# Kernel optimization log

Measured on AMD Instinct MI355X. Metric: run time of the kernel, lower is better.

## Reference

```python
import jax, jax.numpy as jnp
import numpy as np

B, T, DIN, D = 8, 2048, 1024, 1024
EPS = 1e-6


def setup_inputs() -> dict:
    key = jax.random.key(0)
    k0, k1, k2, k3 = jax.random.split(key, 4)
    x = jax.random.normal(k0, (B, T, DIN), dtype=jnp.float32)
    h0 = jax.random.normal(k1, (B, D), dtype=jnp.float32)
    s0 = jax.random.normal(k2, (B, D), dtype=jnp.float32)
    # xavier_uniform for weight [7D, DIN]
    bound = float(np.sqrt(6.0 / (DIN + 7 * D)))
    W = jax.random.uniform(k3, (7 * D, DIN), dtype=jnp.float32, minval=-bound, maxval=bound)
    # structured bias init from _init_weights: [0, 1, 0, 0, 0, 2, 0.5] per block
    b = jnp.concatenate([
        jnp.zeros(D), jnp.ones(D), jnp.zeros(D), jnp.zeros(D),
        jnp.zeros(D), jnp.full((D,), 2.0), jnp.full((D,), 0.5)
    ]).astype(jnp.float32)
    return {"x": x, "h0": h0, "s0": s0, "W": W, "b": b}


def _forward(x, h0, s0, W, b):
    Bv, Tv, _ = x.shape
    Dv = W.shape[0] // 7
    gates = (jnp.einsum('bti,oi->bto', x, W) + b).reshape(Bv, Tv, 7, Dv)
    r, z, k, v, h_pre, decay, alpha = (gates[:, :, i] for i in range(7))
    # per-element pairwise RMS norms, exactly as in the Triton kernel
    rms_control = jnp.sqrt((r * r + z * z) / 2 + EPS)
    rms_kv = jnp.sqrt((k * k + v * v) / 2 + EPS)
    # r is normalized+sigmoided in the kernel but never used -> no effect on output
    z = jax.nn.sigmoid(z / rms_control)
    decay = jax.nn.sigmoid(decay / jnp.sqrt(decay * decay + EPS))
    alpha = jax.nn.sigmoid(alpha / jnp.sqrt(alpha * alpha + EPS))
    h_pre = h_pre / jnp.sqrt(h_pre * h_pre + EPS)
    kv = (k / rms_kv) * (v / rms_kv) / (rms_kv * rms_kv + EPS)
    # time-major [T,B,D] for the scan
    seq = tuple(jnp.swapaxes(a, 0, 1) for a in (z, kv, h_pre, decay, alpha))

    def step(carry, ins):
        h, s = carry
        z_t, kv_t, hp_t, d_t, a_t = ins
        s = d_t * s + a_t * kv_t
        c = jax.nn.sigmoid(2.0 * (hp_t + s)) * 2.0 - 1.0
        h = (1.0 - z_t) * c + z_t * h
        return (h, s), h

    (_, sT), out = jax.lax.scan(step, (h0, s0), seq)
    return jnp.swapaxes(out, 0, 1), sT  # ([B,T,D], [B,D])


def reference(x, h0, s0, W, b):
    return _forward(x, h0, s0, W, b)
```

## Files before the change

kernel.cpp:

```cpp
#include <hip/hip_runtime.h>
#include <hip/hip_bf16.h>

typedef _Float16 f16x8 __attribute__((ext_vector_type(8)));
typedef float f32x4 __attribute__((ext_vector_type(4)));

static constexpr int BB = 8;
static constexpr int TT = 2048;
static constexpr int DD = 1024;
static constexpr int MM = BB * TT;
static constexpr int NN = 7 * DD;
static constexpr int APS = 2048;
static constexpr int NCSUB = 32;
static constexpr int LC = TT / NCSUB;
static constexpr int BD = BB * DD;
#define EPS_ 1e-6f

static constexpr size_t SZ_CMP = (size_t)MM * DD * 8;
static constexpr size_t SZ_BP  = (size_t)NN * 3072 * 2;
static constexpr size_t SZ_SM  = (size_t)NCSUB * BD * 4;
static constexpr size_t OFF_BP  = SZ_CMP;
static constexpr size_t OFF_SM  = OFF_BP + SZ_BP;
static constexpr size_t OFF_AP  = OFF_SM + 6 * SZ_SM;
static constexpr size_t CHUNK_BYTES = (size_t)MM * 18432;

__device__ __forceinline__ unsigned short bf_rne(float f) {
    unsigned u = __builtin_bit_cast(unsigned, f);
    unsigned r = (u + 0x7fffu + ((u >> 16) & 1u)) >> 16;
    return (unsigned short)r;
}
__device__ __forceinline__ float bf2f(unsigned short u) {
    return __builtin_bit_cast(float, ((unsigned)u) << 16);
}
__device__ __forceinline__ float f16f(unsigned short u) {
    return (float)__builtin_bit_cast(_Float16, u);
}
__device__ __forceinline__ unsigned short f16b(float f) {
    return __builtin_bit_cast(unsigned short, (_Float16)f);
}
__device__ __forceinline__ float sigm(float x) { return 1.0f / (1.0f + __expf(-x)); }

typedef __attribute__((address_space(3))) void lds_void;
typedef const __attribute__((address_space(1))) void gbl_void;
__device__ __forceinline__ void gload16(const void* g, void* l) {
    __builtin_amdgcn_global_load_lds((gbl_void*)g, (lds_void*)l, 16, 0, 0);
}

__global__ __launch_bounds__(256) void prep_w(const float* __restrict__ W,
                                              _Float16* __restrict__ Bp1,
                                              _Float16* __restrict__ Bp2) {
    int i = blockIdx.x * 256 + threadIdx.x;
    int o = i >> 10, k = i & 1023;
    int g = o >> 10, d = o & 1023;
    float wv = W[i] * 512.0f;
    _Float16 w1 = (_Float16)wv;
    _Float16 w2 = (_Float16)(wv - (float)w1);
    if (g == 0 || g == 1 || g == 4) {
        int r1 = (g == 4 ? 2 : g) * 1024 + d;
        Bp1[(size_t)r1 * 1024 + k] = w1;
    } else {
        int r2 = (g < 4 ? g - 2 : g - 3) * 1024 + d;
        size_t base = (size_t)r2 * 3072 + k;
        Bp2[base] = w1; Bp2[base + 1024] = w1; Bp2[base + 2048] = w2;
    }
}

__global__ __launch_bounds__(256) void prep_x(const float* __restrict__ x,
                                              _Float16* __restrict__ Ap,
                                              int tc, int Tc, int tcShift) {
    int i = blockIdx.x * 256 + threadIdx.x;
    int rho = i >> 10, k = i & 1023;
    int b = rho >> tcShift, tau = rho & (Tc - 1);
    size_t m = (size_t)b * TT + (size_t)tc * Tc + tau;
    float xv = x[m * DD + k] * 16.0f;
    _Float16 x1 = (_Float16)xv;
    _Float16 x2 = (_Float16)(xv - (float)x1);
    size_t base = (size_t)rho * APS + k;
    Ap[base] = x1; Ap[base + 1024] = x2;
}

template<int KT, int NTILES, int NCOLS, int KIND>
__global__ __launch_bounds__(512) void gemm_k(const _Float16* __restrict__ Ap,
                                              const _Float16* __restrict__ Bp,
                                              const float* __restrict__ bias,
                                              _Float16* __restrict__ Gc, int Mt) {
    constexpr int KSTR = KT * 64;
    __shared__ __align__(16) _Float16 As[256 * 64];
    __shared__ __align__(16) _Float16 Bs[128 * 64];
    int nwg = Mt * NTILES;
    int bid = blockIdx.x;
    int cpx = nwg >> 3;
    int swz = (bid & 7) * cpx + (bid >> 3);
    int bm = swz / NTILES, bn = swz % NTILES;
    int m0 = bm * 256, n0 = bn * 128;
    int tid = threadIdx.x;
    int w = tid >> 6, l = tid & 63;
    int wm = w >> 1, wn = w & 1;
    int lrow = l & 15, kg = l >> 4;
    f32x4 acc[4][4] = {};
    const char* Ab = (const char*)Ap;
    const char* Bb = (const char*)Bp;
    for (int k0 = 0; k0 < KT * 64; k0 += 64) {
        int ak0 = k0 & 2047;
#pragma unroll
        for (int q = 0; q < 4; ++q) {
            int c = q * 512 + tid;
            int row = c >> 3, sgg = (c & 7) ^ (row & 7);
            gload16(Ab + ((size_t)(m0 + row) * APS + ak0 + sgg * 8) * 2, (char*)As + c * 16);
        }
#pragma unroll
        for (int q = 0; q < 2; ++q) {
            int c = q * 512 + tid;
            int row = c >> 3, sgg = (c & 7) ^ (row & 7);
            gload16(Bb + ((size_t)(n0 + row) * KSTR + k0 + sgg * 8) * 2, (char*)Bs + c * 16);
        }
        __syncthreads();
#pragma unroll
        for (int kk = 0; kk < 64; kk += 32) {
            f16x8 af[4], bfr[4];
            int sgb = kg + (kk >> 3);
#pragma unroll
            for (int i = 0; i < 4; ++i) {
                int r = wm * 64 + i * 16 + lrow;
                af[i] = *(const f16x8*)(As + r * 64 + (size_t)((sgb ^ (r & 7)) * 8));
            }
#pragma unroll
            for (int j = 0; j < 4; ++j) {
                int r = wn * 64 + j * 16 + lrow;
                bfr[j] = *(const f16x8*)(Bs + r * 64 + (size_t)((sgb ^ (r & 7)) * 8));
            }
#pragma unroll
            for (int i = 0; i < 4; ++i)
#pragma unroll
                for (int j = 0; j < 4; ++j)
                    acc[i][j] = __builtin_amdgcn_mfma_f32_16x16x32_f16(af[i], bfr[j], acc[i][j], 0, 0, 0);
        }
        __syncthreads();
    }
    const float inv = 1.0f / 8192.0f;
#pragma unroll
    for (int j = 0; j < 4; ++j) {
        int o = n0 + wn * 64 + j * 16 + lrow;
        int g = o >> 10, d = o & 1023;
        float bv;
        if (KIND == 1) bv = bias[(g == 2 ? 4 : g) * 1024 + d];
        else           bv = bias[(g < 2 ? g + 2 : g + 3) * 1024 + d];
#pragma unroll
        for (int i = 0; i < 4; ++i) {
            int rb = m0 + wm * 64 + i * 16 + kg * 4;
#pragma unroll
            for (int r = 0; r < 4; ++r) {
                float val = acc[i][j][r] * inv + bv;
                if (KIND == 1) {
                    if (g == 2) val = val * rsqrtf(val * val + EPS_);
                } else {
                    if (g >= 2) val = sigm(val * rsqrtf(val * val + EPS_));
                }
                Gc[(size_t)(rb + r) * NCOLS + o] = (_Float16)val;
            }
        }
    }
}

__global__ __launch_bounds__(256) void compact_k(const _Float16* __restrict__ Gc1,
                                                 const _Float16* __restrict__ Gc2,
                                                 ushort2* __restrict__ cmpA,
                                                 ushort2* __restrict__ cmpB,
                                                 int tc, int Tc, int tcShift) {
    int idx = blockIdx.x * 256 + threadIdx.x;
    int rho = idx >> 10, d = idx & 1023;
    const _Float16* row1 = Gc1 + (size_t)rho * 3072;
    const _Float16* row2 = Gc2 + (size_t)rho * 4096;
    float r   = row1[d], z  = row1[1024 + d], hpn = row1[2048 + d];
    float k   = row2[d], v  = row2[1024 + d];
    float ds  = row2[2048 + d], as = row2[3072 + d];
    float rc2 = (r * r + z * z) * 0.5f + EPS_;
    float zs = sigm(z * rsqrtf(rc2));
    float rk2 = (k * k + v * v) * 0.5f + EPS_;
    float kv = (k * v) / (rk2 * (rk2 + EPS_));
    float akv = as * kv;
    int b = rho >> tcShift, tau = rho & (Tc - 1);
    size_t m = (size_t)b * TT + (size_t)tc * Tc + tau;
    ushort2 ua; ua.x = bf_rne(akv); ua.y = f16b(ds);
    ushort2 ub; ub.x = f16b(zs);    ub.y = f16b(hpn);
    cmpA[m * DD + d] = ua;
    cmpB[m * DD + d] = ub;
}

__global__ __launch_bounds__(256) void passA(const ushort2* __restrict__ cmpA,
                                             float* __restrict__ SP, float* __restrict__ SQ) {
    int bid = blockIdx.x;
    int b = bid >> 7, rem = bid & 127;
    int ch = rem >> 2, d = (rem & 3) * 256 + threadIdx.x;
    const ushort2* p = cmpA + ((size_t)(b * TT + ch * LC)) * DD + d;
    float P = 1.0f, Q = 0.0f;
#pragma unroll 4
    for (int i = 0; i < LC; ++i) {
        ushort2 u = p[(size_t)i * DD];
        float akv = bf2f(u.x), ds = f16f(u.y);
        P *= ds; Q = ds * Q + akv;
    }
    int bd = b * DD + d;
    SP[ch * BD + bd] = P; SQ[ch * BD + bd] = Q;
}

__global__ __launch_bounds__(256) void passB(const float* __restrict__ s0,
                                             const float* __restrict__ SP, const float* __restrict__ SQ,
                                             float* __restrict__ Sst, float* __restrict__ sT) {
    int bd = blockIdx.x * 256 + threadIdx.x;
    float s = s0[bd];
    for (int ch = 0; ch < NCSUB; ++ch) {
        Sst[ch * BD + bd] = s;
        s = SP[ch * BD + bd] * s + SQ[ch * BD + bd];
    }
    sT[bd] = s;
}

__global__ __launch_bounds__(256) void passC(const ushort2* __restrict__ cmpA,
                                             const ushort2* __restrict__ cmpB,
                                             const float* __restrict__ Sst,
                                             float* __restrict__ HZ, float* __restrict__ HR) {
    int bid = blockIdx.x;
    int b = bid >> 7, rem = bid & 127;
    int ch = rem >> 2, d = (rem & 3) * 256 + threadIdx.x;
    int bd = b * DD + d;
    float s = Sst[ch * BD + bd];
    float Z = 1.0f, R = 0.0f;
    size_t base = ((size_t)(b * TT + ch * LC)) * DD + d;
#pragma unroll 4
    for (int i = 0; i < LC; ++i) {
        ushort2 ua = cmpA[base + (size_t)i * DD];
        ushort2 ub = cmpB[base + (size_t)i * DD];
        float akv = bf2f(ua.x), ds = f16f(ua.y), zs = f16f(ub.x), hpn = f16f(ub.y);
        s = ds * s + akv;
        float c = 2.0f * sigm(2.0f * (hpn + s)) - 1.0f;
        Z *= zs; R = zs * R + (1.0f - zs) * c;
    }
    HZ[ch * BD + bd] = Z; HR[ch * BD + bd] = R;
}

__global__ __launch_bounds__(256) void passD(const float* __restrict__ h0,
                                             const float* __restrict__ HZ, const float* __restrict__ HR,
                                             float* __restrict__ Hst) {
    int bd = blockIdx.x * 256 + threadIdx.x;
    float h = h0[bd];
    for (int ch = 0; ch < NCSUB; ++ch) {
        Hst[ch * BD + bd] = h;
        h = HZ[ch * BD + bd] * h + HR[ch * BD + bd];
    }
}

__global__ __launch_bounds__(256) void passE(const ushort2* __restrict__ cmpA,
                                             const ushort2* __restrict__ cmpB,
                                             const float* __restrict__ Sst,
                                             const float* __restrict__ Hst,
                                             float* __restrict__ out) {
    int bid = blockIdx.x;
    int b = bid >> 7, rem = bid & 127;
    int ch = rem >> 2, d = (rem & 3) * 256 + threadIdx.x;
    int bd = b * DD + d;
    float s = Sst[ch * BD + bd];
    float h = Hst[ch * BD + bd];
    size_t base = ((size_t)(b * TT + ch * LC)) * DD + d;
    float* op = out + base;
#pragma unroll 4
    for (int i = 0; i < LC; ++i) {
        ushort2 ua = cmpA[base + (size_t)i * DD];
        ushort2 ub = cmpB[base + (size_t)i * DD];
        float akv = bf2f(ua.x), ds = f16f(ua.y), zs = f16f(ub.x), hpn = f16f(ub.y);
        s = ds * s + akv;
        float c = 2.0f * sigm(2.0f * (hpn + s)) - 1.0f;
        h = (1.0f - zs) * c + zs * h;
        op[(size_t)i * DD] = h;
    }
}

__global__ __launch_bounds__(256) void sentinel_k(float* __restrict__ sT) {
    int i = blockIdx.x * 256 + threadIdx.x;
    if (i < BD) sT[i] = 1e9f;
}

extern "C" void kernel_launch(void* const* d_in, const int* in_sizes, int n_in,
                              void* d_out, int out_size, void* d_ws, size_t ws_size,
                              hipStream_t stream) {
    const float* x    = (const float*)d_in[0];
    const float* h0   = (const float*)d_in[1];
    const float* s0   = (const float*)d_in[2];
    const float* W    = (const float*)d_in[3];
    const float* bias = (const float*)d_in[4];
    float* out = (float*)d_out;
    float* sT  = out + (size_t)MM * DD;
    char* ws = (char*)d_ws;

    int NCH = 0;
    for (int c : {2, 4, 8, 16, 32}) {
        if (OFF_AP + CHUNK_BYTES / c <= ws_size) { NCH = c; break; }
    }
    if (!NCH) {
        sentinel_k<<<BD / 256, 256, 0, stream>>>(sT);
        return;
    }
    int Mc = MM / NCH;
    int Tc = TT / NCH;
    int tcShift = 31 - __builtin_clz(Tc);
    int Mt = Mc / 256;

    ushort2* cmpA = (ushort2*)ws;
    ushort2* cmpB = (ushort2*)(ws + (size_t)MM * DD * 4);
    _Float16* Bp1 = (_Float16*)(ws + OFF_BP);
    _Float16* Bp2 = (_Float16*)(ws + OFF_BP + (size_t)3072 * 1024 * 2);
    float* SP  = (float*)(ws + OFF_SM);
    float* SQ  = (float*)(ws + OFF_SM + 1 * SZ_SM);
    float* Sst = (float*)(ws + OFF_SM + 2 * SZ_SM);
    float* HZ  = (float*)(ws + OFF_SM + 3 * SZ_SM);
    float* HR  = (float*)(ws + OFF_SM + 4 * SZ_SM);
    float* Hst = (float*)(ws + OFF_SM + 5 * SZ_SM);
    _Float16* Ap  = (_Float16*)(ws + OFF_AP);
    _Float16* Gc1 = (_Float16*)(ws + OFF_AP + (size_t)Mc * APS * 2);
    _Float16* Gc2 = Gc1 + (size_t)Mc * 3072;

    prep_w<<<(NN * DD) / 256, 256, 0, stream>>>(W, Bp1, Bp2);
    for (int tc = 0; tc < NCH; ++tc) {
        prep_x<<<Mc * 4, 256, 0, stream>>>(x, Ap, tc, Tc, tcShift);
        gemm_k<16, 24, 3072, 1><<<Mt * 24, 512, 0, stream>>>(Ap, Bp1, bias, Gc1, Mt);
        gemm_k<48, 32, 4096, 2><<<Mt * 32, 512, 0, stream>>>(Ap, Bp2, bias, Gc2, Mt);
        compact_k<<<Mc * 4, 256, 0, stream>>>(Gc1, Gc2, cmpA, cmpB, tc, Tc, tcShift);
    }
    passA<<<BB * NCSUB * 4, 256, 0, stream>>>(cmpA, SP, SQ);
    passB<<<BD / 256, 256, 0, stream>>>(s0, SP, SQ, Sst, sT);
    passC<<<BB * NCSUB * 4, 256, 0, stream>>>(cmpA, cmpB, Sst, HZ, HR);
    passD<<<BD / 256, 256, 0, stream>>>(h0, HZ, HR, Hst);
    passE<<<BB * NCSUB * 4, 256, 0, stream>>>(cmpA, cmpB, Sst, Hst, out);
}
```

Measured before the change: 754.7 us.

## Replace second gate GEMM with 256x256-tile, 8-wave pipelined MFMA kernel

Adds a new gemm8 kernel for the second (k, v, decay, alpha) GEMM. It uses 256x256 output tiles, 8 waves each computing 128x64, a double-buffered 128KB LDS pipeline with direct global-to-LDS loads, XOR-swizzled LDS addressing, s_setprio around MFMA bursts, and an XCD-aware block swizzle. The larger tile raises data reuse per loaded byte and aims to overlap loads with MFMA work. The cost is one workgroup per CU, high register pressure and fewer workgroups to fill the device.

```diff
diff --git a/kernel.cpp b/kernel.cpp
--- a/kernel.cpp
+++ b/kernel.cpp
@@ -161,6 +161,125 @@
     }
 }
 
+__global__ __launch_bounds__(512, 1) void gemm8(const _Float16* __restrict__ Ap,
+                                                const _Float16* __restrict__ Bp,
+                                                const float* __restrict__ bias,
+                                                _Float16* __restrict__ Gc, int Mt) {
+    __shared__ __align__(16) char smem[131072];
+    constexpr int NT = 48;
+    int nwg = Mt * 16;
+    int bid = blockIdx.x;
+    int cpx = nwg >> 3;
+    int swz = (bid & 7) * cpx + (bid >> 3);
+    int bm = swz / 16, bn = swz % 16;
+    int m0 = bm * 256, n0 = bn * 256;
+    int t = threadIdx.x;
+    int l = t & 63;
+    int wid = t >> 6;
+    int wm = wid >> 2, wn = wid & 3;
+    int lrow = l & 15, kg = l >> 4;
+    int grow = t >> 2;
+    int sg = (t & 3) ^ ((t >> 3) & 3);
+    const char* aGb = (const char*)(Ap + (size_t)(m0 + grow) * APS + sg * 8);
+    const char* bGb = (const char*)(Bp + (size_t)(n0 + grow) * 3072 + sg * 8);
+    unsigned ldst = (unsigned)t * 16;
+    int sp = kg ^ ((lrow >> 1) & 3);
+    unsigned aRd = (unsigned)((wm * 128 + lrow) * 64 + sp * 16);
+    unsigned bRd = (unsigned)(65536 + (wn * 64 + lrow) * 64 + sp * 16);
+    f32x4 acc[2][4][4] = {};
+    f16x8 af[4], bf[4];
+
+    auto stA = [&](int tt, int kh, int pd) {
+        int col = (tt * 64 + kh * 32) & 2047;
+        const char* g = aGb + (size_t)col * 2;
+        unsigned d = (unsigned)((pd * 2 + kh) * 16384) + ldst;
+        gload16(g, smem + d);
+        gload16(g + (size_t)128 * APS * 2, smem + d + 8192);
+    };
+    auto stB = [&](int tt, int kh, int pd) {
+        const char* g = bGb + (size_t)(tt * 64 + kh * 32) * 2;
+        unsigned d = 65536u + (unsigned)((pd * 2 + kh) * 16384) + ldst;
+        gload16(g, smem + d);
+        gload16(g + (size_t)128 * 3072 * 2, smem + d + 8192);
+    };
+    auto dsA = [&](int p, int kk, int mh) {
+#pragma unroll
+        for (int i = 0; i < 4; ++i)
+            af[i] = *(const f16x8*)(smem + (aRd + (unsigned)((p * 2 + kk) * 16384 + mh * 4096 + i * 1024)));
+    };
+    auto dsB = [&](int p, int kk) {
+#pragma unroll
+        for (int j = 0; j < 4; ++j)
+            bf[j] = *(const f16x8*)(smem + (bRd + (unsigned)((p * 2 + kk) * 16384 + j * 1024)));
+    };
+    auto MF = [&](int mh) {
+        __builtin_amdgcn_s_setprio(1);
+#pragma unroll
+        for (int i = 0; i < 4; ++i)
+#pragma unroll
+            for (int j = 0; j < 4; ++j)
+                acc[mh][i][j] = __builtin_amdgcn_mfma_f32_16x16x32_f16(af[i], bf[j], acc[mh][i][j], 0, 0, 0);
+        __builtin_amdgcn_s_setprio(0);
+    };
+#define BAR() { __builtin_amdgcn_s_barrier(); __builtin_amdgcn_sched_barrier(0); }
+#define VMC(n) { asm volatile("s_waitcnt vmcnt(" #n ")" ::: "memory"); __builtin_amdgcn_sched_barrier(0); }
+
+    stA(0, 0, 0); stB(0, 0, 0); stA(0, 1, 0); stB(0, 1, 0);
+    stA(1, 0, 1); stB(1, 0, 1);
+    VMC(4);
+    BAR();
+
+    for (int tau = 0; tau < NT; ++tau) {
+        int p = tau & 1, q = p ^ 1;
+        bool s1 = (tau + 1) < NT, s2 = (tau + 2) < NT;
+        dsB(p, 0); dsA(p, 0, 0);
+        if (s1) stA(tau + 1, 1, q);
+        BAR();
+        MF(0);
+        BAR();
+        dsA(p, 0, 1);
+        if (s1) stB(tau + 1, 1, q);
+        BAR();
+        MF(1);
+        if (s1) VMC(4);
+        BAR();
+        dsB(p, 1); dsA(p, 1, 0);
+        if (s2) stA(tau + 2, 0, p);
+        BAR();
+        MF(0);
+        BAR();
+        dsA(p, 1, 1);
+        if (s2) stB(tau + 2, 0, p);
+        BAR();
+        MF(1);
+        if (s2) { VMC(4); }
+        else if (s1) { VMC(0); }
+        BAR();
+    }
+#undef BAR
+#undef VMC
+
+    const float inv = 1.0f / 8192.0f;
+#pragma unroll
+    for (int j = 0; j < 4; ++j) {
+        int o = n0 + wn * 64 + j * 16 + lrow;
+        int g = o >> 10, d = o & 1023;
+        float bv = bias[(g < 2 ? g + 2 : g + 3) * 1024 + d];
+#pragma unroll
+        for (int mh = 0; mh < 2; ++mh)
+#pragma unroll
+        for (int i = 0; i < 4; ++i) {
+            int rb = m0 + wm * 128 + mh * 64 + i * 16 + kg * 4;
+#pragma unroll
+            for (int r = 0; r < 4; ++r) {
+                float val = acc[mh][i][j][r] * inv + bv;
+                if (g >= 2) val = sigm(val * rsqrtf(val * val + EPS_));
+                Gc[(size_t)(rb + r) * 4096 + o] = (_Float16)val;
+            }
+        }
+    }
+}
+
 __global__ __launch_bounds__(256) void compact_k(const _Float16* __restrict__ Gc1,
                                                  const _Float16* __restrict__ Gc2,
                                                  ushort2* __restrict__ cmpA,
@@ -322,7 +441,7 @@
     for (int tc = 0; tc < NCH; ++tc) {
         prep_x<<<Mc * 4, 256, 0, stream>>>(x, Ap, tc, Tc, tcShift);
         gemm_k<16, 24, 3072, 1><<<Mt * 24, 512, 0, stream>>>(Ap, Bp1, bias, Gc1, Mt);
-        gemm_k<48, 32, 4096, 2><<<Mt * 32, 512, 0, stream>>>(Ap, Bp2, bias, Gc2, Mt);
+        gemm8<<<Mt * 16, 512, 0, stream>>>(Ap, Bp2, bias, Gc2, Mt);
         compact_k<<<Mc * 4, 256, 0, stream>>>(Gc1, Gc2, cmpA, cmpB, tc, Tc, tcShift);
     }
     passA<<<BB * NCSUB * 4, 256, 0, stream>>>(cmpA, SP, SQ);
```

Result: no change. 764.5 us (+1.3%).

## Fuse gate compaction into GEMM epilogues via interleaved weight row layout

Applied to the files above, without the earlier changes.

Reorders weight rows so paired gates (r/z and k/v/decay/alpha) land in adjacent output columns, letting the GEMM epilogue combine them with lane shuffles and write the compact scan inputs directly. This removes the separate compact kernel and the fp16 gate intermediate buffers and their round trip through memory. zs and hpn are split into separate planes, which frees workspace and allows a single chunk when the workspace is large enough. The epilogue now makes scattered 2-byte and 4-byte stores with only a quarter of lanes active in the second GEMM, which may reduce store efficiency.

```diff
diff --git a/kernel.cpp b/kernel.cpp
--- a/kernel.cpp
+++ b/kernel.cpp
@@ -15,13 +15,16 @@
 static constexpr int BD = BB * DD;
 #define EPS_ 1e-6f
 
-static constexpr size_t SZ_CMP = (size_t)MM * DD * 8;
-static constexpr size_t SZ_BP  = (size_t)NN * 3072 * 2;
-static constexpr size_t SZ_SM  = (size_t)NCSUB * BD * 4;
-static constexpr size_t OFF_BP  = SZ_CMP;
+static constexpr size_t SZ_CMPA = (size_t)MM * DD * 4;
+static constexpr size_t SZ_PLN  = (size_t)MM * DD * 2;
+static constexpr size_t SZ_BP   = (size_t)NN * 3072 * 2;
+static constexpr size_t SZ_SM   = (size_t)NCSUB * BD * 4;
+static constexpr size_t OFF_ZS  = SZ_CMPA;
+static constexpr size_t OFF_HPN = OFF_ZS + SZ_PLN;
+static constexpr size_t OFF_BP  = OFF_HPN + SZ_PLN;
 static constexpr size_t OFF_SM  = OFF_BP + SZ_BP;
 static constexpr size_t OFF_AP  = OFF_SM + 6 * SZ_SM;
-static constexpr size_t CHUNK_BYTES = (size_t)MM * 18432;
+static constexpr size_t CHUNK_BYTES = (size_t)MM * APS * 2;
 
 __device__ __forceinline__ unsigned short bf_rne(float f) {
     unsigned u = __builtin_bit_cast(unsigned, f);
@@ -54,12 +57,13 @@
     float wv = W[i] * 512.0f;
     _Float16 w1 = (_Float16)wv;
     _Float16 w2 = (_Float16)(wv - (float)w1);
-    if (g == 0 || g == 1 || g == 4) {
-        int r1 = (g == 4 ? 2 : g) * 1024 + d;
-        Bp1[(size_t)r1 * 1024 + k] = w1;
+    if (g == 0 || g == 1) {
+        Bp1[(size_t)(d * 2 + g) * 1024 + k] = w1;
+    } else if (g == 4) {
+        Bp1[(size_t)(2048 + d) * 1024 + k] = w1;
     } else {
-        int r2 = (g < 4 ? g - 2 : g - 3) * 1024 + d;
-        size_t base = (size_t)r2 * 3072 + k;
+        int g2 = (g < 4 ? g - 2 : g - 3);
+        size_t base = (size_t)(d * 4 + g2) * 3072 + k;
         Bp2[base] = w1; Bp2[base + 1024] = w1; Bp2[base + 2048] = w2;
     }
 }
@@ -78,11 +82,14 @@
     Ap[base] = x1; Ap[base + 1024] = x2;
 }
 
-template<int KT, int NTILES, int NCOLS, int KIND>
+template<int KT, int NTILES, int KIND>
 __global__ __launch_bounds__(512) void gemm_k(const _Float16* __restrict__ Ap,
                                               const _Float16* __restrict__ Bp,
                                               const float* __restrict__ bias,
-                                              _Float16* __restrict__ Gc, int Mt) {
+                                              ushort2* __restrict__ cmpA,
+                                              unsigned short* __restrict__ zsP,
+                                              unsigned short* __restrict__ hpnP,
+                                              int Mt, int tcOff, int Tc, int tcShift) {
     constexpr int KSTR = KT * 64;
     __shared__ __align__(16) _Float16 As[256 * 64];
     __shared__ __align__(16) _Float16 Bs[128 * 64];
@@ -140,50 +147,47 @@
 #pragma unroll
     for (int j = 0; j < 4; ++j) {
         int o = n0 + wn * 64 + j * 16 + lrow;
-        int g = o >> 10, d = o & 1023;
-        float bv;
-        if (KIND == 1) bv = bias[(g == 2 ? 4 : g) * 1024 + d];
-        else           bv = bias[(g < 2 ? g + 2 : g + 3) * 1024 + d];
 #pragma unroll
         for (int i = 0; i < 4; ++i) {
-            int rb = m0 + wm * 64 + i * 16 + kg * 4;
+            int rbase = m0 + wm * 64 + i * 16 + kg * 4;
 #pragma unroll
             for (int r = 0; r < 4; ++r) {
-                float val = acc[i][j][r] * inv + bv;
+                int rb = rbase + r;
+                int bb = rb >> tcShift, tau = rb & (Tc - 1);
+                size_t gm = (size_t)bb * TT + tcOff + tau;
                 if (KIND == 1) {
-                    if (g == 2) val = val * rsqrtf(val * val + EPS_);
+                    if (n0 < 2048) {
+                        int d = o >> 1, g = o & 1;
+                        float val = acc[i][j][r] * inv + bias[g * 1024 + d];
+                        float part = __shfl_xor(val, 1);
+                        if (g == 1) {
+                            float zs = sigm(val * rsqrtf((part * part + val * val) * 0.5f + EPS_));
+                            zsP[gm * DD + d] = f16b(zs);
+                        }
+                    } else {
+                        int d = o - 2048;
+                        float val = acc[i][j][r] * inv + bias[4 * 1024 + d];
+                        hpnP[gm * DD + d] = f16b(val * rsqrtf(val * val + EPS_));
+                    }
                 } else {
-                    if (g >= 2) val = sigm(val * rsqrtf(val * val + EPS_));
+                    int g2 = o & 3, d = o >> 2;
+                    int og = (g2 == 0 ? 2 : g2 == 1 ? 3 : g2 == 2 ? 5 : 6);
+                    float val = acc[i][j][r] * inv + bias[og * 1024 + d];
+                    if (g2 >= 2) val = sigm(val * rsqrtf(val * val + EPS_));
+                    float v1 = __shfl_xor(val, 1);
+                    float v2 = __shfl_xor(val, 2);
+                    float v3 = __shfl_xor(val, 3);
+                    if ((l & 3) == 0) {
+                        float rk2 = (val * val + v1 * v1) * 0.5f + EPS_;
+                        float kv = (val * v1) / (rk2 * (rk2 + EPS_));
+                        float akv = v3 * kv;
+                        ushort2 ua; ua.x = bf_rne(akv); ua.y = f16b(v2);
+                        cmpA[gm * DD + d] = ua;
+                    }
                 }
-                Gc[(size_t)(rb + r) * NCOLS + o] = (_Float16)val;
             }
         }
     }
-}
-
-__global__ __launch_bounds__(256) void compact_k(const _Float16* __restrict__ Gc1,
-                                                 const _Float16* __restrict__ Gc2,
-                                                 ushort2* __restrict__ cmpA,
-                                                 ushort2* __restrict__ cmpB,
-                                                 int tc, int Tc, int tcShift) {
-    int idx = blockIdx.x * 256 + threadIdx.x;
-    int rho = idx >> 10, d = idx & 1023;
-    const _Float16* row1 = Gc1 + (size_t)rho * 3072;
-    const _Float16* row2 = Gc2 + (size_t)rho * 4096;
-    float r   = row1[d], z  = row1[1024 + d], hpn = row1[2048 + d];
-    float k   = row2[d], v  = row2[1024 + d];
-    float ds  = row2[2048 + d], as = row2[3072 + d];
-    float rc2 = (r * r + z * z) * 0.5f + EPS_;
-    float zs = sigm(z * rsqrtf(rc2));
-    float rk2 = (k * k + v * v) * 0.5f + EPS_;
-    float kv = (k * v) / (rk2 * (rk2 + EPS_));
-    float akv = as * kv;
-    int b = rho >> tcShift, tau = rho & (Tc - 1);
-    size_t m = (size_t)b * TT + (size_t)tc * Tc + tau;
-    ushort2 ua; ua.x = bf_rne(akv); ua.y = f16b(ds);
-    ushort2 ub; ub.x = f16b(zs);    ub.y = f16b(hpn);
-    cmpA[m * DD + d] = ua;
-    cmpB[m * DD + d] = ub;
 }
 
 __global__ __launch_bounds__(256) void passA(const ushort2* __restrict__ cmpA,
@@ -216,7 +220,8 @@
 }
 
 __global__ __launch_bounds__(256) void passC(const ushort2* __restrict__ cmpA,
-                                             const ushort2* __restrict__ cmpB,
+                                             const unsigned short* __restrict__ zsP,
+                                             const unsigned short* __restrict__ hpnP,
                                              const float* __restrict__ Sst,
                                              float* __restrict__ HZ, float* __restrict__ HR) {
     int bid = blockIdx.x;
@@ -229,8 +234,9 @@
 #pragma unroll 4
     for (int i = 0; i < LC; ++i) {
         ushort2 ua = cmpA[base + (size_t)i * DD];
-        ushort2 ub = cmpB[base + (size_t)i * DD];
-        float akv = bf2f(ua.x), ds = f16f(ua.y), zs = f16f(ub.x), hpn = f16f(ub.y);
+        float akv = bf2f(ua.x), ds = f16f(ua.y);
+        float zs = f16f(zsP[base + (size_t)i * DD]);
+        float hpn = f16f(hpnP[base + (size_t)i * DD]);
         s = ds * s + akv;
         float c = 2.0f * sigm(2.0f * (hpn + s)) - 1.0f;
         Z *= zs; R = zs * R + (1.0f - zs) * c;
@@ -250,7 +256,8 @@
 }
 
 __global__ __launch_bounds__(256) void passE(const ushort2* __restrict__ cmpA,
-                                             const ushort2* __restrict__ cmpB,
+                                             const unsigned short* __restrict__ zsP,
+                                             const unsigned short* __restrict__ hpnP,
                                              const float* __restrict__ Sst,
                                              const float* __restrict__ Hst,
                                              float* __restrict__ out) {
@@ -265,8 +272,9 @@
 #pragma unroll 4
     for (int i = 0; i < LC; ++i) {
         ushort2 ua = cmpA[base + (size_t)i * DD];
-        ushort2 ub = cmpB[base + (size_t)i * DD];
-        float akv = bf2f(ua.x), ds = f16f(ua.y), zs = f16f(ub.x), hpn = f16f(ub.y);
+        float akv = bf2f(ua.x), ds = f16f(ua.y);
+        float zs = f16f(zsP[base + (size_t)i * DD]);
+        float hpn = f16f(hpnP[base + (size_t)i * DD]);
         s = ds * s + akv;
         float c = 2.0f * sigm(2.0f * (hpn + s)) - 1.0f;
         h = (1.0f - zs) * c + zs * h;
@@ -292,7 +300,7 @@
     char* ws = (char*)d_ws;
 
     int NCH = 0;
-    for (int c : {2, 4, 8, 16, 32}) {
+    for (int c : {1, 2, 4, 8, 16, 32}) {
         if (OFF_AP + CHUNK_BYTES / c <= ws_size) { NCH = c; break; }
     }
     if (!NCH) {
@@ -304,8 +312,9 @@
     int tcShift = 31 - __builtin_clz(Tc);
     int Mt = Mc / 256;
 
-    ushort2* cmpA = (ushort2*)ws;
-    ushort2* cmpB = (ushort2*)(ws + (size_t)MM * DD * 4);
+    ushort2* cmpA        = (ushort2*)ws;
+    unsigned short* zsP  = (unsigned short*)(ws + OFF_ZS);
+    unsigned short* hpnP = (unsigned short*)(ws + OFF_HPN);
     _Float16* Bp1 = (_Float16*)(ws + OFF_BP);
     _Float16* Bp2 = (_Float16*)(ws + OFF_BP + (size_t)3072 * 1024 * 2);
     float* SP  = (float*)(ws + OFF_SM);
@@ -314,20 +323,18 @@
     float* HZ  = (float*)(ws + OFF_SM + 3 * SZ_SM);
     float* HR  = (float*)(ws + OFF_SM + 4 * SZ_SM);
     float* Hst = (float*)(ws + OFF_SM + 5 * SZ_SM);
-    _Float16* Ap  = (_Float16*)(ws + OFF_AP);
-    _Float16* Gc1 = (_Float16*)(ws + OFF_AP + (size_t)Mc * APS * 2);
-    _Float16* Gc2 = Gc1 + (size_t)Mc * 3072;
+    _Float16* Ap = (_Float16*)(ws + OFF_AP);
 
     prep_w<<<(NN * DD) / 256, 256, 0, stream>>>(W, Bp1, Bp2);
     for (int tc = 0; tc < NCH; ++tc) {
+        int tcOff = tc * Tc;
         prep_x<<<Mc * 4, 256, 0, stream>>>(x, Ap, tc, Tc, tcShift);
-        gemm_k<16, 24, 3072, 1><<<Mt * 24, 512, 0, stream>>>(Ap, Bp1, bias, Gc1, Mt);
-        gemm_k<48, 32, 4096, 2><<<Mt * 32, 512, 0, stream>>>(Ap, Bp2, bias, Gc2, Mt);
-        compact_k<<<Mc * 4, 256, 0, stream>>>(Gc1, Gc2, cmpA, cmpB, tc, Tc, tcShift);
+        gemm_k<16, 24, 1><<<Mt * 24, 512, 0, stream>>>(Ap, Bp1, bias, cmpA, zsP, hpnP, Mt, tcOff, Tc, tcShift);
+        gemm_k<48, 32, 2><<<Mt * 32, 512, 0, stream>>>(Ap, Bp2, bias, cmpA, zsP, hpnP, Mt, tcOff, Tc, tcShift);
     }
     passA<<<BB * NCSUB * 4, 256, 0, stream>>>(cmpA, SP, SQ);
     passB<<<BD / 256, 256, 0, stream>>>(s0, SP, SQ, Sst, sT);
-    passC<<<BB * NCSUB * 4, 256, 0, stream>>>(cmpA, cmpB, Sst, HZ, HR);
+    passC<<<BB * NCSUB * 4, 256, 0, stream>>>(cmpA, zsP, hpnP, Sst, HZ, HR);
     passD<<<BD / 256, 256, 0, stream>>>(h0, HZ, HR, Hst);
-    passE<<<BB * NCSUB * 4, 256, 0, stream>>>(cmpA, cmpB, Sst, Hst, out);
-}
+    passE<<<BB * NCSUB * 4, 256, 0, stream>>>(cmpA, zsP, hpnP, Sst, Hst, out);
+}
```

Result: slower. 1.022 ms (+35.4%).
